# Kernel optimization log

Measured on AMD Instinct MI355X. Metric: run time of the kernel, lower is better.

## Reference

```python
import jax, jax.numpy as jnp
import numpy as np

NUM_CLASSES = 81
THRESHOLD = 0.5
NEGPOS_RATIO = 3
OBJ_SCORE = 0.01
VAR0, VAR1 = 0.1, 0.2


def point_form(boxes):
    # center form (cx,cy,w,h) -> corner form (x1,y1,x2,y2)
    return jnp.concatenate([boxes[:, :2] - boxes[:, 2:] / 2,
                            boxes[:, :2] + boxes[:, 2:] / 2], axis=1)


def jaccard(a, b):
    # a: [A,4] corners, b: [B,4] corners -> IoU [A,B]
    lt = jnp.maximum(a[:, None, :2], b[None, :, :2])
    rb = jnp.minimum(a[:, None, 2:], b[None, :, 2:])
    wh = jnp.clip(rb - lt, 0.0)
    inter = wh[..., 0] * wh[..., 1]
    area_a = ((a[:, 2] - a[:, 0]) * (a[:, 3] - a[:, 1]))[:, None]
    area_b = ((b[:, 2] - b[:, 0]) * (b[:, 3] - b[:, 1]))[None, :]
    return inter / (area_a + area_b - inter)


def encode(matched, priors):
    # matched: [P,4] corner-form GT, priors: [P,4] center-form
    g_cxcy = ((matched[:, :2] + matched[:, 2:]) / 2 - priors[:, :2]) / (VAR0 * priors[:, 2:])
    g_wh = jnp.log((matched[:, 2:] - matched[:, :2]) / priors[:, 2:]) / VAR1
    return jnp.concatenate([g_cxcy, g_wh], axis=1)


def match_one(truths, labels, priors):
    # truths: [O,4] corners, labels: [O] int, priors: [P,4] center-form
    overlaps = jaccard(truths, point_form(priors))      # [O,P]
    best_prior_idx = jnp.argmax(overlaps, axis=1)       # [O]
    best_truth_overlap = jnp.max(overlaps, axis=0)      # [P]
    best_truth_idx = jnp.argmax(overlaps, axis=0)       # [P]
    # ensure every gt matches its best prior
    best_truth_overlap = best_truth_overlap.at[best_prior_idx].set(2.0)
    best_truth_idx = best_truth_idx.at[best_prior_idx].set(jnp.arange(truths.shape[0]))
    matches = truths[best_truth_idx]                    # [P,4]
    conf = jnp.where(best_truth_overlap < THRESHOLD, 0, labels[best_truth_idx].astype(jnp.int32))
    return encode(matches, priors), conf


def smooth_l1(x):
    ax = jnp.abs(x)
    return jnp.where(ax < 1.0, 0.5 * ax * ax, ax - 0.5)


def ce_per_row(logits, tgt):
    # sum-reduction cross-entropy components: logsumexp - logit[target]
    lse = jax.nn.logsumexp(logits, axis=-1)
    picked = jnp.take_along_axis(logits, tgt[..., None].astype(jnp.int32), axis=-1)[..., 0]
    return lse - picked


def setup_inputs() -> dict:
    key = jax.random.key(0)
    ks = jax.random.split(key, 8)
    B, P, O, C = 32, 24564, 16, NUM_CLASSES
    loc_data = jax.random.normal(ks[0], (B, P, 4), jnp.float32)
    conf_data = jax.random.normal(ks[1], (B, P, C), jnp.float32)
    obj_data = jax.random.normal(ks[2], (B, P, 2), jnp.float32)
    # priors in center form
    pc = jax.random.uniform(ks[3], (P, 2), jnp.float32, 0.0, 1.0)
    pwh = jax.random.uniform(ks[4], (P, 2), jnp.float32, 0.05, 0.5)
    priors = jnp.concatenate([pc, pwh], axis=1)
    # gt boxes in corner form, valid (x1<x2, y1<y2)
    tc = jax.random.uniform(ks[5], (B, O, 2), jnp.float32, 0.2, 0.8)
    twh = jax.random.uniform(ks[6], (B, O, 2), jnp.float32, 0.05, 0.3)
    truths = jnp.concatenate([jnp.clip(tc - twh / 2, 0.0, 1.0),
                              jnp.clip(tc + twh / 2, 0.0, 1.0)], axis=-1)
    labels = jax.random.randint(ks[7], (B, O), 1, C).astype(jnp.int64)
    return {"loc_data": loc_data, "conf_data": conf_data, "obj_data": obj_data,
            "priors": priors, "truths": truths, "labels": labels}


def reference(loc_data, conf_data, obj_data, priors, truths, labels):
    num, num_priors = loc_data.shape[:2]
    loc_t, conf_t = jax.vmap(match_one, in_axes=(0, 0, None))(truths, labels, priors)
    loc_t = jax.lax.stop_gradient(loc_t)      # Variable(requires_grad=False)
    conf_t = jax.lax.stop_gradient(conf_t)
    obj_t = (conf_t > 0).astype(jnp.int32)

    obj_conf = jax.lax.stop_gradient(obj_data[:, :, 1])   # .detach()
    pos = conf_t > 0
    # faithful to original (buggy) filter: (pos + neg_positive) > 2 is never true
    neg_positive = (pos.astype(jnp.int32) + (obj_conf < OBJ_SCORE).astype(jnp.int32)) > 2
    pos = pos & ~neg_positive
    pos = jnp.where(pos.sum() == 0, conf_t > 0, pos)

    # localization loss (smooth L1, sum over positives)
    l1 = smooth_l1(loc_data - loc_t).sum(-1)               # [B,P]
    loss_l = jnp.sum(jnp.where(pos, l1, 0.0))

    # objectness loss with hard negative mining
    ce_obj = ce_per_row(obj_data, obj_t)                   # [B,P]
    pos_obj = obj_t > 0
    mining_obj = jnp.where(pos_obj, 0.0, jax.lax.stop_gradient(ce_obj))
    rank_obj = jnp.argsort(jnp.argsort(-mining_obj, axis=1), axis=1)
    num_obj_pos = pos_obj.sum(1, keepdims=True)
    num_obj_neg = jnp.minimum(NEGPOS_RATIO * num_obj_pos, num_priors - 1)
    neg_obj = rank_obj < num_obj_neg
    loss_obj = jnp.sum(jnp.where(pos_obj | neg_obj, ce_obj, 0.0))

    # class confidence loss with hard negative mining
    ce_c = ce_per_row(conf_data, conf_t)                   # [B,P]
    mining_c = jnp.where(pos, 0.0, jax.lax.stop_gradient(ce_c))
    rank_c = jnp.argsort(jnp.argsort(-mining_c, axis=1), axis=1)
    num_pos = pos.sum(1, keepdims=True)
    num_neg = jnp.minimum(NEGPOS_RATIO * num_pos, num_priors - 1)
    neg = rank_c < num_neg
    loss_c = jnp.sum(jnp.where(pos | neg, ce_c, 0.0))

    N = jnp.maximum(num_pos.sum(), 1).astype(loc_data.dtype)
    N1 = jnp.maximum(num_obj_neg.sum(), 1).astype(loc_data.dtype)
    return (loss_l / N, loss_c / N, 0.4 * loss_obj / N1)
```

## Files before the change

### kernel.cpp

```cpp
#include <hip/hip_runtime.h>
#include <hip/hip_bf16.h>
#include <math.h>

#define BB 32
#define PP 24564
#define OO 16
#define CC 81
#define BP (BB * PP)
#define CHUNK 1024

typedef unsigned long long ull;

__device__ __forceinline__ float sl1(float x) {
    float ax = fabsf(x);
    return ax < 1.0f ? 0.5f * ax * ax : ax - 0.5f;
}

__global__ __launch_bounds__(256) void k_match_a(
        const float* __restrict__ priors, const float* __restrict__ truths,
        ull* __restrict__ best_prior ) {
    const int b = blockIdx.y;
    const int p0 = blockIdx.x * CHUNK;
    const int tid = threadIdx.x;
    __shared__ float tr[OO][4];
    __shared__ float tarea[OO];
    __shared__ ull red[4][OO];
    if (tid < OO * 4) ((float*)tr)[tid] = truths[b * OO * 4 + tid];
    __syncthreads();
    if (tid < OO) tarea[tid] = (tr[tid][2] - tr[tid][0]) * (tr[tid][3] - tr[tid][1]);
    __syncthreads();

    float bpv[OO];
    int bpi[OO];
#pragma unroll
    for (int o = 0; o < OO; o++) { bpv[o] = -1.0f; bpi[o] = -1; }

    const int pend = (p0 + CHUNK < PP) ? p0 + CHUNK : PP;
    for (int p = p0 + tid; p < pend; p += 256) {
        const float4 pr = ((const float4*)priors)[p];
        const float x1 = pr.x - pr.z * 0.5f, y1 = pr.y - pr.w * 0.5f;
        const float x2 = pr.x + pr.z * 0.5f, y2 = pr.y + pr.w * 0.5f;
        const float parea = (x2 - x1) * (y2 - y1);
#pragma unroll
        for (int o = 0; o < OO; o++) {
            const float lx = fmaxf(tr[o][0], x1), ly = fmaxf(tr[o][1], y1);
            const float rx = fminf(tr[o][2], x2), ry = fminf(tr[o][3], y2);
            const float iw = fmaxf(rx - lx, 0.0f), ih = fmaxf(ry - ly, 0.0f);
            const float inter = iw * ih;
            const float iou = inter / (tarea[o] + parea - inter);
            if (iou > bpv[o]) { bpv[o] = iou; bpi[o] = p; }
        }
    }

    const int wave = tid >> 6;
    const int lane = tid & 63;
#pragma unroll
    for (int o = 0; o < OO; o++) {
        ull key = (bpi[o] >= 0)
            ? (((ull)__float_as_uint(bpv[o]) << 32) |
               (ull)(0xFFFFFFFFu - (unsigned)bpi[o]))
            : 0ull;
#pragma unroll
        for (int d = 32; d; d >>= 1) {
            const ull other = __shfl_xor(key, d);
            key = (other > key) ? other : key;
        }
        if (lane == 0) red[wave][o] = key;
    }
    __syncthreads();
    if (tid < OO) {
        const ull k0 = red[0][tid], k1 = red[1][tid];
        const ull k2 = red[2][tid], k3 = red[3][tid];
        ull m = k0 > k1 ? k0 : k1;
        const ull m2 = k2 > k3 ? k2 : k3;
        m = m > m2 ? m : m2;
        if (m != 0ull) atomicMax(&best_prior[b * OO + tid], m);
    }
}

__global__ __launch_bounds__(256) void k_ce(
        const float* __restrict__ conf, const float* __restrict__ obj,
        const float* __restrict__ loc, const float* __restrict__ priors,
        const float* __restrict__ truths, const int* __restrict__ labels,
        const ull* __restrict__ best_prior,
        float* __restrict__ mining_obj, float* __restrict__ mining_c,
        int* __restrict__ num_posS ,
        float* __restrict__ accS  ) {
    const int tid = threadIdx.x;
    const int row0 = blockIdx.x * 64;
    const int b0 = row0 / PP;
    __shared__ float sconf[64 * CC];
    __shared__ float slse[64];
    __shared__ float4 s_tr[2][OO];
    __shared__ float  s_ta[2][OO];
    __shared__ int    s_lb[2][OO];
    __shared__ unsigned s_fp[2][OO];

    const int nb = ((row0 - b0 * PP) + 64 > PP) ? 2 : 1;
    if (tid < nb * OO) {
        const int bb = tid >> 4, o = tid & 15;
        const float4 t = ((const float4*)truths)[(b0 + bb) * OO + o];
        s_tr[bb][o] = t;
        s_ta[bb][o] = (t.z - t.x) * (t.w - t.y);
        s_lb[bb][o] = labels[(b0 + bb) * OO + o];
        s_fp[bb][o] = 0xFFFFFFFFu -
            (unsigned)(best_prior[(b0 + bb) * OO + o] & 0xFFFFFFFFull);
    }

    const float4* src = (const float4*)(conf + (size_t)row0 * CC);
    float4* dst = (float4*)sconf;
    for (int i = tid; i < (64 * CC) / 4; i += 256) dst[i] = src[i];
    __syncthreads();

    const int r = tid >> 2;
    const int part = tid & 3;
    const float* rowp = sconf + r * CC;
    const int c0 = part * 20;
    const int c1 = (part == 3) ? CC : c0 + 20;
    float m = -INFINITY;
    for (int c = c0; c < c1; c++) m = fmaxf(m, rowp[c]);
    m = fmaxf(m, __shfl_xor(m, 1));
    m = fmaxf(m, __shfl_xor(m, 2));
    float s = 0.0f;
    for (int c = c0; c < c1; c++) s += __expf(rowp[c] - m);
    s += __shfl_xor(s, 1);
    s += __shfl_xor(s, 2);
    if (part == 0) slse[r] = m + __logf(s);
    __syncthreads();

    if (tid < 64) {
        const int row = row0 + tid;
        const int b = row / PP;
        const int lb_i = b - b0;
        const int p = row - b * PP;

        const float4 pr = ((const float4*)priors)[p];
        const float x1 = pr.x - pr.z * 0.5f, y1 = pr.y - pr.w * 0.5f;
        const float x2 = pr.x + pr.z * 0.5f, y2 = pr.y + pr.w * 0.5f;
        const float parea = (x2 - x1) * (y2 - y1);
        float best = -1.0f;
        int ti = 0;
#pragma unroll
        for (int o = 0; o < OO; o++) {
            const float4 t = s_tr[lb_i][o];
            const float lx = fmaxf(t.x, x1), ly = fmaxf(t.y, y1);
            const float rx = fminf(t.z, x2), ry = fminf(t.w, y2);
            const float iw = fmaxf(rx - lx, 0.0f), ih = fmaxf(ry - ly, 0.0f);
            const float inter = iw * ih;
            const float iou = inter / (s_ta[lb_i][o] + parea - inter);
            if (iou > best) { best = iou; ti = o; }
        }
        float ov = best;
#pragma unroll
        for (int o = 0; o < OO; o++) {
            if (s_fp[lb_i][o] == (unsigned)p) { ti = o; ov = 2.0f; }
        }

        const int lbl = s_lb[lb_i][ti];
        const int tgt = (ov < 0.5f) ? 0 : lbl;
        const float ce_c = slse[tid] - sconf[tid * CC + tgt];

        const float2 o2 = ((const float2*)obj)[row];
        const float mo = fmaxf(o2.x, o2.y);
        const float lse_o = mo + __logf(__expf(o2.x - mo) + __expf(o2.y - mo));
        const bool pos = tgt > 0;
        const float ce_o = lse_o - (pos ? o2.y : o2.x);

        mining_c[row]   = pos ? 0.0f : ce_c;
        mining_obj[row] = pos ? 0.0f : ce_o;

        float my_l = 0.0f, my_co = 0.0f, my_cc = 0.0f;
        if (pos) {
            my_co = ce_o;
            my_cc = ce_c;
            const float4 t = s_tr[lb_i][ti];
            const float gcx = ((t.x + t.z) * 0.5f - pr.x) / (0.1f * pr.z);
            const float gcy = ((t.y + t.w) * 0.5f - pr.y) / (0.1f * pr.w);
            const float gw = logf((t.z - t.x) / pr.z) / 0.2f;
            const float gh = logf((t.w - t.y) / pr.w) / 0.2f;
            const float4 ld = ((const float4*)loc)[row];
            my_l = sl1(ld.x - gcx) + sl1(ld.y - gcy) +
                   sl1(ld.z - gw) + sl1(ld.w - gh);
        }

        const ull mpos = __ballot(pos);
        const ull mb1  = __ballot(b != b0);
#pragma unroll
        for (int d = 32; d; d >>= 1) {
            my_l  += __shfl_down(my_l,  d);
            my_co += __shfl_down(my_co, d);
            my_cc += __shfl_down(my_cc, d);
        }
        if (tid == 0 && mpos) {
            const int cnt0 = __popcll(mpos & ~mb1);
            const int cnt1 = __popcll(mpos &  mb1);
            int* nps = num_posS + (blockIdx.x & 7) * BB;
            if (cnt0) atomicAdd(&nps[b0], cnt0);
            if (cnt1) atomicAdd(&nps[b0 + 1], cnt1);
            float* slot = accS + (size_t)(blockIdx.x & 63) * 32;
            atomicAdd(slot + 0, my_l);
            atomicAdd(slot + 1, my_co);
            atomicAdd(slot + 2, my_cc);
        }
    }
}

__global__ __launch_bounds__(1024) void k_select(
        const float* __restrict__ mining ,
        const int* __restrict__ num_posS ,
        float* __restrict__ acc,
        int* __restrict__ n1_acc) {
    const int arr = blockIdx.x >> 5;
    const int b = blockIdx.x & 31;
    const int tid = threadIdx.x;
    const int wv = tid >> 6;
    const float* x = mining + ((size_t)arr * BB + b) * PP;
    int np = 0;
#pragma unroll
    for (int s = 0; s < 8; s++) np += num_posS[s * BB + b];
    long long k64 = 3LL * np;
    const int k = (int)(k64 < (long long)(PP - 1) ? k64 : (long long)(PP - 1));
    if (tid == 0 && arr == 0) atomicAdd(n1_acc, k);
    if (k <= 0) return;

    __shared__ unsigned histw[16][256];
    __shared__ unsigned hist[256];
    __shared__ unsigned s_prefix;
    __shared__ int s_krem;
    __shared__ float wsum[16];
    __shared__ unsigned wcnt[16];
    if (tid == 0) { s_prefix = 0u; s_krem = k; }

    for (int shift = 24; shift >= 0; shift -= 8) {
        __syncthreads();
        for (int i = tid; i < 16 * 256; i += 1024) ((unsigned*)histw)[i] = 0u;
        const unsigned prefix = s_prefix;
        const unsigned pmask = (shift == 24) ? 0u : (0xFFFFFFFFu << (shift + 8));
        __syncthreads();
        for (int i = tid; i < PP; i += 1024) {
            const unsigned u = __float_as_uint(x[i]);
            if ((u & pmask) == prefix)
                atomicAdd(&histw[wv][(u >> shift) & 255u], 1u);
        }
        __syncthreads();
        if (tid < 256) {
            unsigned s = 0;
#pragma unroll
            for (int w = 0; w < 16; w++) s += histw[w][tid];
            hist[tid] = s;
        }
        __syncthreads();
        if (tid == 0) {
            const int krem = s_krem;
            unsigned cum = 0;
            int sel = 0;
            for (int byte = 255; byte >= 0; byte--) {
                const unsigned h = hist[byte];
                if (cum + h >= (unsigned)krem) { sel = byte; break; }
                cum += h;
            }
            s_krem = krem - (int)cum;
            s_prefix = prefix | ((unsigned)sel << shift);
        }
    }
    __syncthreads();

    const unsigned t = s_prefix;
    float lsum = 0.0f;
    unsigned lcnt = 0;
    for (int i = tid; i < PP; i += 1024) {
        const float v = x[i];
        if (__float_as_uint(v) > t) { lsum += v; lcnt++; }
    }
#pragma unroll
    for (int d = 32; d; d >>= 1) {
        lsum += __shfl_down(lsum, d);
        lcnt += __shfl_down(lcnt, d);
    }
    if ((tid & 63) == 0) { wsum[wv] = lsum; wcnt[wv] = lcnt; }
    __syncthreads();
    if (tid == 0) {
        float ts = 0.0f;
        unsigned tc = 0;
#pragma unroll
        for (int w = 0; w < 16; w++) { ts += wsum[w]; tc += wcnt[w]; }
        const float tsum = ts + (float)(k - (int)tc) * __uint_as_float(t);
        atomicAdd(&acc[3 + arr], tsum);
    }
}

__global__ void k_final(const float* __restrict__ acc,
                        const float* __restrict__ accS ,
                        const int* __restrict__ num_posS ,
                        const int* __restrict__ n1_acc,
                        float* __restrict__ out) {
    const int t = threadIdx.x;
    float sl = accS[t * 32 + 0];
    float so = accS[t * 32 + 1];
    float sc = accS[t * 32 + 2];
    int np = 0;
#pragma unroll
    for (int i = 0; i < 4; i++) np += num_posS[t + i * 64];
#pragma unroll
    for (int d = 32; d; d >>= 1) {
        sl += __shfl_down(sl, d);
        so += __shfl_down(so, d);
        sc += __shfl_down(sc, d);
        np += __shfl_down(np, d);
    }
    if (t == 0) {
        const float fN = (float)(np > 1 ? np : 1);
        const int n1 = *n1_acc;
        const float fN1 = (float)(n1 > 1 ? n1 : 1);
        out[0] = sl / fN;
        out[1] = (sc + acc[4]) / fN;
        out[2] = 0.4f * (so + acc[3]) / fN1;
    }
}

extern "C" void kernel_launch(void* const* d_in, const int* in_sizes, int n_in,
                              void* d_out, int out_size, void* d_ws, size_t ws_size,
                              hipStream_t stream) {
    const float* loc_data  = (const float*)d_in[0];
    const float* conf_data = (const float*)d_in[1];
    const float* obj_data  = (const float*)d_in[2];
    const float* priors    = (const float*)d_in[3];
    const float* truths    = (const float*)d_in[4];
    const int*   labels    = (const int*)d_in[5];
    float* out = (float*)d_out;

    float* ws_f = (float*)d_ws;
    float* mining = ws_f;
    ull*   best_prior = (ull*)(ws_f + 2 * (size_t)BP);
    int*   num_posS = (int*)(ws_f + 2 * (size_t)BP + 1024);
    float* acc = ws_f + 2 * (size_t)BP + 1280;
    int*   n1_acc = (int*)(ws_f + 2 * (size_t)BP + 1288);
    float* accS = ws_f + 2 * (size_t)BP + 2048;

    hipMemsetAsync((void*)best_prior, 0, 16384, stream);

    dim3 mg((PP + CHUNK - 1) / CHUNK, BB);
    k_match_a<<<mg, 256, 0, stream>>>(priors, truths, best_prior);

    k_ce<<<BP / 64, 256, 0, stream>>>(conf_data, obj_data, loc_data, priors,
                                      truths, labels, best_prior,
                                      mining , mining + BP ,
                                      num_posS, accS);

    k_select<<<64, 1024, 0, stream>>>(mining, num_posS, acc, n1_acc);

    k_final<<<1, 64, 0, stream>>>(acc, accS, num_posS, n1_acc, out);
}
```

Measured before the change: 464.7 us.

## Fuse all loss stages into one persistent cooperative kernel with grid syncs

Replaces the four separate launches (match, CE, select, final) with a single cooperative persistent kernel that uses grid.sync between phases. The CE phase now loads conf rows straight into registers instead of staging them in shared memory. The top-k radix select is spread across many blocks using a global histogram and state, where it used to run in only 64 blocks of 1024 threads. This removes launch gaps and the underutilised select phase, at the cost of grid-wide barriers, a larger memset, and lower per-block occupancy limits.

```diff
diff --git a/kernel.cpp b/kernel.cpp
--- a/kernel.cpp
+++ b/kernel.cpp
@@ -1,6 +1,8 @@
 #include <hip/hip_runtime.h>
-#include <hip/hip_bf16.h>
+#include <hip/hip_cooperative_groups.h>
 #include <math.h>
+
+namespace cg = cooperative_groups;
 
 #define BB 32
 #define PP 24564
@@ -8,6 +10,10 @@
 #define CC 81
 #define BP (BB * PP)
 #define CHUNK 1024
+#define NCHK ((PP + CHUNK - 1) / CHUNK)
+#define NMATCH (NCHK * BB)
+#define NTILE (BP / 64)
+#define NSB 512
 
 typedef unsigned long long ull;
 
@@ -16,305 +22,374 @@
     return ax < 1.0f ? 0.5f * ax * ax : ax - 0.5f;
 }
 
-__global__ __launch_bounds__(256) void k_match_a(
-        const float* __restrict__ priors, const float* __restrict__ truths,
-        ull* __restrict__ best_prior ) {
-    const int b = blockIdx.y;
-    const int p0 = blockIdx.x * CHUNK;
-    const int tid = threadIdx.x;
-    __shared__ float tr[OO][4];
-    __shared__ float tarea[OO];
-    __shared__ ull red[4][OO];
-    if (tid < OO * 4) ((float*)tr)[tid] = truths[b * OO * 4 + tid];
-    __syncthreads();
-    if (tid < OO) tarea[tid] = (tr[tid][2] - tr[tid][0]) * (tr[tid][3] - tr[tid][1]);
-    __syncthreads();
-
-    float bpv[OO];
-    int bpi[OO];
-#pragma unroll
-    for (int o = 0; o < OO; o++) { bpv[o] = -1.0f; bpi[o] = -1; }
-
-    const int pend = (p0 + CHUNK < PP) ? p0 + CHUNK : PP;
-    for (int p = p0 + tid; p < pend; p += 256) {
-        const float4 pr = ((const float4*)priors)[p];
-        const float x1 = pr.x - pr.z * 0.5f, y1 = pr.y - pr.w * 0.5f;
-        const float x2 = pr.x + pr.z * 0.5f, y2 = pr.y + pr.w * 0.5f;
-        const float parea = (x2 - x1) * (y2 - y1);
-#pragma unroll
-        for (int o = 0; o < OO; o++) {
-            const float lx = fmaxf(tr[o][0], x1), ly = fmaxf(tr[o][1], y1);
-            const float rx = fminf(tr[o][2], x2), ry = fminf(tr[o][3], y2);
-            const float iw = fmaxf(rx - lx, 0.0f), ih = fmaxf(ry - ly, 0.0f);
-            const float inter = iw * ih;
-            const float iou = inter / (tarea[o] + parea - inter);
-            if (iou > bpv[o]) { bpv[o] = iou; bpi[o] = p; }
-        }
-    }
-
-    const int wave = tid >> 6;
-    const int lane = tid & 63;
-#pragma unroll
-    for (int o = 0; o < OO; o++) {
-        ull key = (bpi[o] >= 0)
-            ? (((ull)__float_as_uint(bpv[o]) << 32) |
-               (ull)(0xFFFFFFFFu - (unsigned)bpi[o]))
-            : 0ull;
-#pragma unroll
-        for (int d = 32; d; d >>= 1) {
-            const ull other = __shfl_xor(key, d);
-            key = (other > key) ? other : key;
-        }
-        if (lane == 0) red[wave][o] = key;
-    }
-    __syncthreads();
-    if (tid < OO) {
-        const ull k0 = red[0][tid], k1 = red[1][tid];
-        const ull k2 = red[2][tid], k3 = red[3][tid];
-        ull m = k0 > k1 ? k0 : k1;
-        const ull m2 = k2 > k3 ? k2 : k3;
-        m = m > m2 ? m : m2;
-        if (m != 0ull) atomicMax(&best_prior[b * OO + tid], m);
-    }
-}
-
-__global__ __launch_bounds__(256) void k_ce(
+__device__ __forceinline__ float4 ld4u(const float* p) {
+    float4 v;
+    __builtin_memcpy(&v, p, 16);
+    return v;
+}
+
+__device__ __forceinline__ float ald(const float* p) {
+    return __hip_atomic_load(p, __ATOMIC_RELAXED, __HIP_MEMORY_SCOPE_AGENT);
+}
+__device__ __forceinline__ int aldi(const int* p) {
+    return __hip_atomic_load(p, __ATOMIC_RELAXED, __HIP_MEMORY_SCOPE_AGENT);
+}
+
+__global__ __launch_bounds__(256, 4) void k_mega(
         const float* __restrict__ conf, const float* __restrict__ obj,
         const float* __restrict__ loc, const float* __restrict__ priors,
         const float* __restrict__ truths, const int* __restrict__ labels,
-        const ull* __restrict__ best_prior,
-        float* __restrict__ mining_obj, float* __restrict__ mining_c,
-        int* __restrict__ num_posS ,
-        float* __restrict__ accS  ) {
+        ull* __restrict__ best_prior,
+        float* __restrict__ mining,
+        int* __restrict__ num_posS,
+        float* __restrict__ acc,
+        float* __restrict__ accS,
+        unsigned* __restrict__ ghist,
+        ull* __restrict__ gstate,
+        float* __restrict__ out) {
     const int tid = threadIdx.x;
-    const int row0 = blockIdx.x * 64;
-    const int b0 = row0 / PP;
-    __shared__ float sconf[64 * CC];
-    __shared__ float slse[64];
-    __shared__ float4 s_tr[2][OO];
-    __shared__ float  s_ta[2][OO];
-    __shared__ int    s_lb[2][OO];
-    __shared__ unsigned s_fp[2][OO];
-
-    const int nb = ((row0 - b0 * PP) + 64 > PP) ? 2 : 1;
-    if (tid < nb * OO) {
-        const int bb = tid >> 4, o = tid & 15;
-        const float4 t = ((const float4*)truths)[(b0 + bb) * OO + o];
-        s_tr[bb][o] = t;
-        s_ta[bb][o] = (t.z - t.x) * (t.w - t.y);
-        s_lb[bb][o] = labels[(b0 + bb) * OO + o];
-        s_fp[bb][o] = 0xFFFFFFFFu -
-            (unsigned)(best_prior[(b0 + bb) * OO + o] & 0xFFFFFFFFull);
-    }
-
-    const float4* src = (const float4*)(conf + (size_t)row0 * CC);
-    float4* dst = (float4*)sconf;
-    for (int i = tid; i < (64 * CC) / 4; i += 256) dst[i] = src[i];
-    __syncthreads();
-
-    const int r = tid >> 2;
-    const int part = tid & 3;
-    const float* rowp = sconf + r * CC;
-    const int c0 = part * 20;
-    const int c1 = (part == 3) ? CC : c0 + 20;
-    float m = -INFINITY;
-    for (int c = c0; c < c1; c++) m = fmaxf(m, rowp[c]);
-    m = fmaxf(m, __shfl_xor(m, 1));
-    m = fmaxf(m, __shfl_xor(m, 2));
-    float s = 0.0f;
-    for (int c = c0; c < c1; c++) s += __expf(rowp[c] - m);
-    s += __shfl_xor(s, 1);
-    s += __shfl_xor(s, 2);
-    if (part == 0) slse[r] = m + __logf(s);
-    __syncthreads();
-
-    if (tid < 64) {
-        const int row = row0 + tid;
+    const int bid = blockIdx.x;
+    const int nblk = gridDim.x;
+    cg::grid_group grid = cg::this_grid();
+
+    __shared__ float s_tr[OO][4];
+    __shared__ float s_ta[OO];
+    __shared__ ull s_red[4][OO];
+    __shared__ unsigned s_histw[4][256];
+    __shared__ unsigned s_bins[256];
+    __shared__ float s_ws[4];
+    __shared__ unsigned s_wc[4];
+
+    for (int task = bid; task < NMATCH; task += nblk) {
+        const int b = task / NCHK;
+        const int c = task - b * NCHK;
+        __syncthreads();
+        if (tid < OO * 4) ((float*)s_tr)[tid] = truths[b * OO * 4 + tid];
+        __syncthreads();
+        if (tid < OO)
+            s_ta[tid] = (s_tr[tid][2] - s_tr[tid][0]) * (s_tr[tid][3] - s_tr[tid][1]);
+        __syncthreads();
+
+        float bpv[OO];
+        int bpi[OO];
+#pragma unroll
+        for (int o = 0; o < OO; o++) { bpv[o] = -1.0f; bpi[o] = -1; }
+
+        const int p0 = c * CHUNK;
+        const int pend = (p0 + CHUNK < PP) ? p0 + CHUNK : PP;
+        for (int p = p0 + tid; p < pend; p += 256) {
+            const float4 pr = ((const float4*)priors)[p];
+            const float x1 = pr.x - pr.z * 0.5f, y1 = pr.y - pr.w * 0.5f;
+            const float x2 = pr.x + pr.z * 0.5f, y2 = pr.y + pr.w * 0.5f;
+            const float parea = (x2 - x1) * (y2 - y1);
+#pragma unroll
+            for (int o = 0; o < OO; o++) {
+                const float lx = fmaxf(s_tr[o][0], x1), ly = fmaxf(s_tr[o][1], y1);
+                const float rx = fminf(s_tr[o][2], x2), ry = fminf(s_tr[o][3], y2);
+                const float iw = fmaxf(rx - lx, 0.0f), ih = fmaxf(ry - ly, 0.0f);
+                const float inter = iw * ih;
+                const float iou = inter / (s_ta[o] + parea - inter);
+                if (iou > bpv[o]) { bpv[o] = iou; bpi[o] = p; }
+            }
+        }
+
+        const int wave = tid >> 6;
+        const int lane = tid & 63;
+#pragma unroll
+        for (int o = 0; o < OO; o++) {
+            ull key = (bpi[o] >= 0)
+                ? (((ull)__float_as_uint(bpv[o]) << 32) |
+                   (ull)(0xFFFFFFFFu - (unsigned)bpi[o]))
+                : 0ull;
+#pragma unroll
+            for (int d = 32; d; d >>= 1) {
+                const ull other = __shfl_xor(key, d);
+                key = (other > key) ? other : key;
+            }
+            if (lane == 0) s_red[wave][o] = key;
+        }
+        __syncthreads();
+        if (tid < OO) {
+            const ull k0 = s_red[0][tid], k1 = s_red[1][tid];
+            const ull k2 = s_red[2][tid], k3 = s_red[3][tid];
+            ull m = k0 > k1 ? k0 : k1;
+            const ull m2 = k2 > k3 ? k2 : k3;
+            m = m > m2 ? m : m2;
+            if (m != 0ull) atomicMax(&best_prior[b * OO + tid], m);
+        }
+    }
+
+    __threadfence();
+    grid.sync();
+
+    for (int tile = bid; tile < NTILE; tile += nblk) {
+        const int row0 = tile * 64;
+        const int r = tid >> 2;
+        const int part = tid & 3;
+        const int row = row0 + r;
+        const float* rowp = conf + (size_t)row * CC;
+        const int c0 = part * 20;
+
+        const float4 v0 = ld4u(rowp + c0);
+        const float4 v1 = ld4u(rowp + c0 + 4);
+        const float4 v2 = ld4u(rowp + c0 + 8);
+        const float4 v3 = ld4u(rowp + c0 + 12);
+        const float4 v4 = ld4u(rowp + c0 + 16);
+        const float ex = (part == 3) ? rowp[80] : 0.0f;
+
+        float m = v0.x;
+        m = fmaxf(m, v0.y); m = fmaxf(m, v0.z); m = fmaxf(m, v0.w);
+        m = fmaxf(m, v1.x); m = fmaxf(m, v1.y); m = fmaxf(m, v1.z); m = fmaxf(m, v1.w);
+        m = fmaxf(m, v2.x); m = fmaxf(m, v2.y); m = fmaxf(m, v2.z); m = fmaxf(m, v2.w);
+        m = fmaxf(m, v3.x); m = fmaxf(m, v3.y); m = fmaxf(m, v3.z); m = fmaxf(m, v3.w);
+        m = fmaxf(m, v4.x); m = fmaxf(m, v4.y); m = fmaxf(m, v4.z); m = fmaxf(m, v4.w);
+        if (part == 3) m = fmaxf(m, ex);
+        m = fmaxf(m, __shfl_xor(m, 1));
+        m = fmaxf(m, __shfl_xor(m, 2));
+
+        float s = 0.0f;
+        s += __expf(v0.x - m); s += __expf(v0.y - m); s += __expf(v0.z - m); s += __expf(v0.w - m);
+        s += __expf(v1.x - m); s += __expf(v1.y - m); s += __expf(v1.z - m); s += __expf(v1.w - m);
+        s += __expf(v2.x - m); s += __expf(v2.y - m); s += __expf(v2.z - m); s += __expf(v2.w - m);
+        s += __expf(v3.x - m); s += __expf(v3.y - m); s += __expf(v3.z - m); s += __expf(v3.w - m);
+        s += __expf(v4.x - m); s += __expf(v4.y - m); s += __expf(v4.z - m); s += __expf(v4.w - m);
+        if (part == 3) s += __expf(ex - m);
+        s += __shfl_xor(s, 1);
+        s += __shfl_xor(s, 2);
+        const float lse = m + __logf(s);
+
         const int b = row / PP;
-        const int lb_i = b - b0;
-        const int p = row - b * PP;
-
-        const float4 pr = ((const float4*)priors)[p];
-        const float x1 = pr.x - pr.z * 0.5f, y1 = pr.y - pr.w * 0.5f;
-        const float x2 = pr.x + pr.z * 0.5f, y2 = pr.y + pr.w * 0.5f;
-        const float parea = (x2 - x1) * (y2 - y1);
-        float best = -1.0f;
-        int ti = 0;
-#pragma unroll
-        for (int o = 0; o < OO; o++) {
-            const float4 t = s_tr[lb_i][o];
-            const float lx = fmaxf(t.x, x1), ly = fmaxf(t.y, y1);
-            const float rx = fminf(t.z, x2), ry = fminf(t.w, y2);
-            const float iw = fmaxf(rx - lx, 0.0f), ih = fmaxf(ry - ly, 0.0f);
-            const float inter = iw * ih;
-            const float iou = inter / (s_ta[lb_i][o] + parea - inter);
-            if (iou > best) { best = iou; ti = o; }
-        }
-        float ov = best;
-#pragma unroll
-        for (int o = 0; o < OO; o++) {
-            if (s_fp[lb_i][o] == (unsigned)p) { ti = o; ov = 2.0f; }
-        }
-
-        const int lbl = s_lb[lb_i][ti];
-        const int tgt = (ov < 0.5f) ? 0 : lbl;
-        const float ce_c = slse[tid] - sconf[tid * CC + tgt];
-
-        const float2 o2 = ((const float2*)obj)[row];
-        const float mo = fmaxf(o2.x, o2.y);
-        const float lse_o = mo + __logf(__expf(o2.x - mo) + __expf(o2.y - mo));
-        const bool pos = tgt > 0;
-        const float ce_o = lse_o - (pos ? o2.y : o2.x);
-
-        mining_c[row]   = pos ? 0.0f : ce_c;
-        mining_obj[row] = pos ? 0.0f : ce_o;
-
+        bool pos = false;
         float my_l = 0.0f, my_co = 0.0f, my_cc = 0.0f;
-        if (pos) {
-            my_co = ce_o;
-            my_cc = ce_c;
-            const float4 t = s_tr[lb_i][ti];
-            const float gcx = ((t.x + t.z) * 0.5f - pr.x) / (0.1f * pr.z);
-            const float gcy = ((t.y + t.w) * 0.5f - pr.y) / (0.1f * pr.w);
-            const float gw = logf((t.z - t.x) / pr.z) / 0.2f;
-            const float gh = logf((t.w - t.y) / pr.w) / 0.2f;
-            const float4 ld = ((const float4*)loc)[row];
-            my_l = sl1(ld.x - gcx) + sl1(ld.y - gcy) +
-                   sl1(ld.z - gw) + sl1(ld.w - gh);
-        }
-
+        if (part == 0) {
+            const int p = row - b * PP;
+            const float4 pr = ((const float4*)priors)[p];
+            const float x1 = pr.x - pr.z * 0.5f, y1 = pr.y - pr.w * 0.5f;
+            const float x2 = pr.x + pr.z * 0.5f, y2 = pr.y + pr.w * 0.5f;
+            const float parea = (x2 - x1) * (y2 - y1);
+            float best = -1.0f;
+            int ti = 0;
+            const float4* trb = (const float4*)truths + b * OO;
+#pragma unroll
+            for (int o = 0; o < OO; o++) {
+                const float4 t = trb[o];
+                const float ta = (t.z - t.x) * (t.w - t.y);
+                const float lx = fmaxf(t.x, x1), ly = fmaxf(t.y, y1);
+                const float rx = fminf(t.z, x2), ry = fminf(t.w, y2);
+                const float iw = fmaxf(rx - lx, 0.0f), ih = fmaxf(ry - ly, 0.0f);
+                const float inter = iw * ih;
+                const float iou = inter / (ta + parea - inter);
+                if (iou > best) { best = iou; ti = o; }
+            }
+            float ov = best;
+#pragma unroll
+            for (int o = 0; o < OO; o++) {
+                const unsigned fp = 0xFFFFFFFFu -
+                    (unsigned)(best_prior[b * OO + o] & 0xFFFFFFFFull);
+                if (fp == (unsigned)p) { ti = o; ov = 2.0f; }
+            }
+
+            const int lbl = labels[b * OO + ti];
+            const int tgt = (ov < 0.5f) ? 0 : lbl;
+            const float ce_c = lse - rowp[tgt];
+
+            const float2 o2 = ((const float2*)obj)[row];
+            const float mo = fmaxf(o2.x, o2.y);
+            const float lse_o = mo + __logf(__expf(o2.x - mo) + __expf(o2.y - mo));
+            pos = tgt > 0;
+            const float ce_o = lse_o - (pos ? o2.y : o2.x);
+
+            mining[BP + row] = pos ? 0.0f : ce_c;
+            mining[row]      = pos ? 0.0f : ce_o;
+
+            if (pos) {
+                my_co = ce_o;
+                my_cc = ce_c;
+                const float4 t = trb[ti];
+                const float gcx = ((t.x + t.z) * 0.5f - pr.x) / (0.1f * pr.z);
+                const float gcy = ((t.y + t.w) * 0.5f - pr.y) / (0.1f * pr.w);
+                const float gw = logf((t.z - t.x) / pr.z) / 0.2f;
+                const float gh = logf((t.w - t.y) / pr.w) / 0.2f;
+                const float4 ld = ((const float4*)loc)[row];
+                my_l = sl1(ld.x - gcx) + sl1(ld.y - gcy) +
+                       sl1(ld.z - gw) + sl1(ld.w - gh);
+            }
+        }
+
+        const int lane = tid & 63;
+        const int w = tid >> 6;
         const ull mpos = __ballot(pos);
-        const ull mb1  = __ballot(b != b0);
+        const int bw0 = __shfl(b, 0);
+        const ull mb1 = __ballot(b != bw0);
 #pragma unroll
         for (int d = 32; d; d >>= 1) {
             my_l  += __shfl_down(my_l,  d);
             my_co += __shfl_down(my_co, d);
             my_cc += __shfl_down(my_cc, d);
         }
-        if (tid == 0 && mpos) {
+        if (lane == 0 && mpos) {
+            const int stripe = tile * 4 + w;
             const int cnt0 = __popcll(mpos & ~mb1);
             const int cnt1 = __popcll(mpos &  mb1);
-            int* nps = num_posS + (blockIdx.x & 7) * BB;
-            if (cnt0) atomicAdd(&nps[b0], cnt0);
-            if (cnt1) atomicAdd(&nps[b0 + 1], cnt1);
-            float* slot = accS + (size_t)(blockIdx.x & 63) * 32;
+            int* nps = num_posS + (stripe & 15) * BB;
+            if (cnt0) atomicAdd(&nps[bw0], cnt0);
+            if (cnt1) atomicAdd(&nps[bw0 + 1], cnt1);
+            float* slot = accS + (size_t)(stripe & 127) * 32;
             atomicAdd(slot + 0, my_l);
             atomicAdd(slot + 1, my_co);
             atomicAdd(slot + 2, my_cc);
         }
     }
-}
-
-__global__ __launch_bounds__(1024) void k_select(
-        const float* __restrict__ mining ,
-        const int* __restrict__ num_posS ,
-        float* __restrict__ acc,
-        int* __restrict__ n1_acc) {
-    const int arr = blockIdx.x >> 5;
-    const int b = blockIdx.x & 31;
-    const int tid = threadIdx.x;
-    const int wv = tid >> 6;
-    const float* x = mining + ((size_t)arr * BB + b) * PP;
-    int np = 0;
-#pragma unroll
-    for (int s = 0; s < 8; s++) np += num_posS[s * BB + b];
-    long long k64 = 3LL * np;
-    const int k = (int)(k64 < (long long)(PP - 1) ? k64 : (long long)(PP - 1));
-    if (tid == 0 && arr == 0) atomicAdd(n1_acc, k);
-    if (k <= 0) return;
-
-    __shared__ unsigned histw[16][256];
-    __shared__ unsigned hist[256];
-    __shared__ unsigned s_prefix;
-    __shared__ int s_krem;
-    __shared__ float wsum[16];
-    __shared__ unsigned wcnt[16];
-    if (tid == 0) { s_prefix = 0u; s_krem = k; }
-
-    for (int shift = 24; shift >= 0; shift -= 8) {
-        __syncthreads();
-        for (int i = tid; i < 16 * 256; i += 1024) ((unsigned*)histw)[i] = 0u;
-        const unsigned prefix = s_prefix;
-        const unsigned pmask = (shift == 24) ? 0u : (0xFFFFFFFFu << (shift + 8));
-        __syncthreads();
-        for (int i = tid; i < PP; i += 1024) {
-            const unsigned u = __float_as_uint(x[i]);
-            if ((u & pmask) == prefix)
-                atomicAdd(&histw[wv][(u >> shift) & 255u], 1u);
-        }
-        __syncthreads();
-        if (tid < 256) {
-            unsigned s = 0;
-#pragma unroll
-            for (int w = 0; w < 16; w++) s += histw[w][tid];
-            hist[tid] = s;
-        }
+
+    __threadfence();
+    grid.sync();
+
+    for (int pass = 0; pass < 4; pass++) {
+        const int shift = 24 - pass * 8;
+        for (int sb = bid; sb < NSB; sb += nblk) {
+            const int task = sb >> 3, sub = sb & 7;
+            const int arr = task >> 5, b = task & 31;
+            unsigned prefix = 0;
+            bool active = true;
+            if (pass > 0) {
+                const ull st = gstate[((pass - 1) & 1) * 64 + task];
+                prefix = (unsigned)(st >> 32);
+                if ((int)(st & 0xFFFFFFFFull) <= 0) active = false;
+            }
+            __syncthreads();
+            for (int i = tid; i < 1024; i += 256) ((unsigned*)s_histw)[i] = 0u;
+            __syncthreads();
+            if (active) {
+                const float* x = mining + ((size_t)arr * BB + b) * PP;
+                const unsigned pmask = (pass == 0) ? 0u : (0xFFFFFFFFu << (shift + 8));
+                const int wv = tid >> 6;
+#pragma unroll
+                for (int j = 0; j < 12; j++) {
+                    const int i = j * 2048 + sub * 256 + tid;
+                    if (i < PP) {
+                        const unsigned u = __float_as_uint(x[i]);
+                        if ((u & pmask) == prefix)
+                            atomicAdd(&s_histw[wv][(u >> shift) & 255u], 1u);
+                    }
+                }
+            }
+            __syncthreads();
+            {
+                const unsigned sum = s_histw[0][tid & 255] + s_histw[1][tid & 255] +
+                                     s_histw[2][tid & 255] + s_histw[3][tid & 255];
+                if (sum) atomicAdd(&ghist[((size_t)pass * 64 + task) * 256 + (tid & 255)], sum);
+            }
+        }
+        __threadfence();
+        grid.sync();
+        for (int sb = bid; sb < NSB; sb += nblk) {
+            const int task = sb >> 3;
+            __syncthreads();
+            s_bins[tid & 255] = ghist[((size_t)pass * 64 + task) * 256 + (tid & 255)];
+            __syncthreads();
+            if (tid == 0) {
+                int krem;
+                unsigned prefix;
+                if (pass == 0) {
+                    const int b = task & 31;
+                    int np = 0;
+#pragma unroll
+                    for (int s2 = 0; s2 < 16; s2++) np += aldi(&num_posS[s2 * BB + b]);
+                    long long k64 = 3LL * np;
+                    krem = (int)(k64 < (long long)(PP - 1) ? k64 : (long long)(PP - 1));
+                    prefix = 0u;
+                } else {
+                    const ull st = gstate[((pass - 1) & 1) * 64 + task];
+                    prefix = (unsigned)(st >> 32);
+                    krem = (int)(st & 0xFFFFFFFFull);
+                }
+                if (krem > 0) {
+                    unsigned cum = 0;
+                    int sel = 0;
+                    for (int byte = 255; byte >= 0; byte--) {
+                        const unsigned h = s_bins[byte];
+                        if (cum + h >= (unsigned)krem) { sel = byte; break; }
+                        cum += h;
+                    }
+                    krem -= (int)cum;
+                    prefix |= (unsigned)sel << shift;
+                }
+                gstate[(pass & 1) * 64 + task] = ((ull)prefix << 32) | (unsigned)krem;
+            }
+        }
+        __syncthreads();
+    }
+    for (int sb = bid; sb < NSB; sb += nblk) {
+        const int task = sb >> 3, sub = sb & 7;
+        const int arr = task >> 5, b = task & 31;
+        int np = 0;
+#pragma unroll
+        for (int s2 = 0; s2 < 16; s2++) np += aldi(&num_posS[s2 * BB + b]);
+        long long k64 = 3LL * np;
+        const int k = (int)(k64 < (long long)(PP - 1) ? k64 : (long long)(PP - 1));
+        if (k <= 0) continue;
+        const unsigned t = (unsigned)(gstate[64 + task] >> 32);
+        const float tf = __uint_as_float(t);
+        const float* x = mining + ((size_t)arr * BB + b) * PP;
+        float lsum = 0.0f;
+        unsigned lcnt = 0;
+#pragma unroll
+        for (int j = 0; j < 12; j++) {
+            const int i = j * 2048 + sub * 256 + tid;
+            if (i < PP) {
+                const float v = x[i];
+                if (__float_as_uint(v) > t) { lsum += v; lcnt++; }
+            }
+        }
+#pragma unroll
+        for (int d = 32; d; d >>= 1) {
+            lsum += __shfl_down(lsum, d);
+            lcnt += __shfl_down(lcnt, d);
+        }
+        const int wv = tid >> 6;
+        __syncthreads();
+        if ((tid & 63) == 0) { s_ws[wv] = lsum; s_wc[wv] = lcnt; }
         __syncthreads();
         if (tid == 0) {
-            const int krem = s_krem;
-            unsigned cum = 0;
-            int sel = 0;
-            for (int byte = 255; byte >= 0; byte--) {
-                const unsigned h = hist[byte];
-                if (cum + h >= (unsigned)krem) { sel = byte; break; }
-                cum += h;
-            }
-            s_krem = krem - (int)cum;
-            s_prefix = prefix | ((unsigned)sel << shift);
-        }
-    }
-    __syncthreads();
-
-    const unsigned t = s_prefix;
-    float lsum = 0.0f;
-    unsigned lcnt = 0;
-    for (int i = tid; i < PP; i += 1024) {
-        const float v = x[i];
-        if (__float_as_uint(v) > t) { lsum += v; lcnt++; }
-    }
-#pragma unroll
-    for (int d = 32; d; d >>= 1) {
-        lsum += __shfl_down(lsum, d);
-        lcnt += __shfl_down(lcnt, d);
-    }
-    if ((tid & 63) == 0) { wsum[wv] = lsum; wcnt[wv] = lcnt; }
-    __syncthreads();
-    if (tid == 0) {
-        float ts = 0.0f;
-        unsigned tc = 0;
-#pragma unroll
-        for (int w = 0; w < 16; w++) { ts += wsum[w]; tc += wcnt[w]; }
-        const float tsum = ts + (float)(k - (int)tc) * __uint_as_float(t);
-        atomicAdd(&acc[3 + arr], tsum);
-    }
-}
-
-__global__ void k_final(const float* __restrict__ acc,
-                        const float* __restrict__ accS ,
-                        const int* __restrict__ num_posS ,
-                        const int* __restrict__ n1_acc,
-                        float* __restrict__ out) {
-    const int t = threadIdx.x;
-    float sl = accS[t * 32 + 0];
-    float so = accS[t * 32 + 1];
-    float sc = accS[t * 32 + 2];
-    int np = 0;
-#pragma unroll
-    for (int i = 0; i < 4; i++) np += num_posS[t + i * 64];
-#pragma unroll
-    for (int d = 32; d; d >>= 1) {
-        sl += __shfl_down(sl, d);
-        so += __shfl_down(so, d);
-        sc += __shfl_down(sc, d);
-        np += __shfl_down(np, d);
-    }
-    if (t == 0) {
-        const float fN = (float)(np > 1 ? np : 1);
-        const int n1 = *n1_acc;
-        const float fN1 = (float)(n1 > 1 ? n1 : 1);
-        out[0] = sl / fN;
-        out[1] = (sc + acc[4]) / fN;
-        out[2] = 0.4f * (so + acc[3]) / fN1;
+            float ts = s_ws[0] + s_ws[1] + s_ws[2] + s_ws[3];
+            const unsigned tc = s_wc[0] + s_wc[1] + s_wc[2] + s_wc[3];
+            float part = ts - (float)(int)tc * tf;
+            if (sub == 0) part += (float)k * tf;
+            atomicAdd(&acc[3 + arr], part);
+        }
+    }
+
+    __threadfence();
+    grid.sync();
+
+    if (bid == 0 && tid < 64) {
+        float sl = ald(&accS[tid * 32 + 0]) + ald(&accS[(tid + 64) * 32 + 0]);
+        float so = ald(&accS[tid * 32 + 1]) + ald(&accS[(tid + 64) * 32 + 1]);
+        float sc = ald(&accS[tid * 32 + 2]) + ald(&accS[(tid + 64) * 32 + 2]);
+        int np_b = 0, k_b = 0;
+        if (tid < BB) {
+#pragma unroll
+            for (int s2 = 0; s2 < 16; s2++) np_b += aldi(&num_posS[s2 * BB + tid]);
+            long long k64 = 3LL * np_b;
+            k_b = (int)(k64 < (long long)(PP - 1) ? k64 : (long long)(PP - 1));
+        }
+#pragma unroll
+        for (int d = 32; d; d >>= 1) {
+            sl += __shfl_down(sl, d);
+            so += __shfl_down(so, d);
+            sc += __shfl_down(sc, d);
+            np_b += __shfl_down(np_b, d);
+            k_b  += __shfl_down(k_b,  d);
+        }
+        if (tid == 0) {
+            const float fN = (float)(np_b > 1 ? np_b : 1);
+            const float fN1 = (float)(k_b > 1 ? k_b : 1);
+            const float a3 = ald(&acc[3]);
+            const float a4 = ald(&acc[4]);
+            out[0] = sl / fN;
+            out[1] = (sc + a4) / fN;
+            out[2] = 0.4f * (so + a3) / fN1;
+        }
     }
 }
 
@@ -331,23 +406,39 @@
 
     float* ws_f = (float*)d_ws;
     float* mining = ws_f;
-    ull*   best_prior = (ull*)(ws_f + 2 * (size_t)BP);
-    int*   num_posS = (int*)(ws_f + 2 * (size_t)BP + 1024);
-    float* acc = ws_f + 2 * (size_t)BP + 1280;
-    int*   n1_acc = (int*)(ws_f + 2 * (size_t)BP + 1288);
-    float* accS = ws_f + 2 * (size_t)BP + 2048;
-
-    hipMemsetAsync((void*)best_prior, 0, 16384, stream);
-
-    dim3 mg((PP + CHUNK - 1) / CHUNK, BB);
-    k_match_a<<<mg, 256, 0, stream>>>(priors, truths, best_prior);
-
-    k_ce<<<BP / 64, 256, 0, stream>>>(conf_data, obj_data, loc_data, priors,
-                                      truths, labels, best_prior,
-                                      mining , mining + BP ,
-                                      num_posS, accS);
-
-    k_select<<<64, 1024, 0, stream>>>(mining, num_posS, acc, n1_acc);
-
-    k_final<<<1, 64, 0, stream>>>(acc, accS, num_posS, n1_acc, out);
-}
+    const size_t S = 2 * (size_t)BP;
+    ull*      best_prior = (ull*)(ws_f + S);
+    int*      num_posS   = (int*)(ws_f + S + 1024);
+    float*    acc        = ws_f + S + 1536;
+    float*    accS       = ws_f + S + 2048;
+    unsigned* ghist      = (unsigned*)(ws_f + S + 6144);
+    ull*      gstate     = (ull*)(ws_f + S + 71680);
+
+    hipMemsetAsync((void*)best_prior, 0, 287744, stream);
+
+    static int s_grid = 0;
+    if (s_grid == 0) {
+        int nb = 0;
+        if (hipOccupancyMaxActiveBlocksPerMultiprocessor(&nb, k_mega, 256, 0)
+                != hipSuccess || nb < 1)
+            nb = 2;
+        int ncu = 256;
+        int dev = 0;
+        hipDeviceProp_t prop;
+        if (hipGetDevice(&dev) == hipSuccess &&
+            hipGetDeviceProperties(&prop, dev) == hipSuccess &&
+            prop.multiProcessorCount > 0)
+            ncu = prop.multiProcessorCount;
+        long long g = (long long)nb * (long long)ncu;
+        s_grid = (int)(g < 1024 ? g : 1024);
+    }
+
+    void* args[] = {
+        (void*)&conf_data, (void*)&obj_data, (void*)&loc_data, (void*)&priors,
+        (void*)&truths, (void*)&labels, (void*)&best_prior, (void*)&mining,
+        (void*)&num_posS, (void*)&acc, (void*)&accS, (void*)&ghist,
+        (void*)&gstate, (void*)&out
+    };
+    hipLaunchCooperativeKernel((void*)k_mega, dim3(s_grid), dim3(256),
+                               args, 0, stream);
+}
```

Result: slower. 1.183 ms (+154.6%).

## Fuse final reduction into select via last-block counter and drop memset

Applied to the files above, without the earlier changes.

Matching now runs one 1024-thread block per batch image, so each block writes its best-prior keys directly and the atomicMax plus hipMemsetAsync are no longer needed. Block 0 of the match kernel zeroes the workspace counters instead. The separate final kernel is folded into the select kernel through a done-counter, where the last block to finish does the final reduction. This removes a memset and one launch but leaves only 32 blocks for matching, which lowers parallelism in that stage.

```diff
diff --git a/kernel.cpp b/kernel.cpp
--- a/kernel.cpp
+++ b/kernel.cpp
@@ -7,7 +7,6 @@
 #define OO 16
 #define CC 81
 #define BP (BB * PP)
-#define CHUNK 1024
 
 typedef unsigned long long ull;
 
@@ -16,15 +15,27 @@
     return ax < 1.0f ? 0.5f * ax * ax : ax - 0.5f;
 }
 
-__global__ __launch_bounds__(256) void k_match_a(
+__device__ __forceinline__ float ald(const float* p) {
+    return __hip_atomic_load(p, __ATOMIC_RELAXED, __HIP_MEMORY_SCOPE_AGENT);
+}
+__device__ __forceinline__ int aldi(const int* p) {
+    return __hip_atomic_load(p, __ATOMIC_RELAXED, __HIP_MEMORY_SCOPE_AGENT);
+}
+
+__global__ __launch_bounds__(1024) void k_match(
         const float* __restrict__ priors, const float* __restrict__ truths,
-        ull* __restrict__ best_prior ) {
-    const int b = blockIdx.y;
-    const int p0 = blockIdx.x * CHUNK;
+        ull* __restrict__ best_prior ,
+        float* __restrict__ zero_base ) {
+    const int b = blockIdx.x;
     const int tid = threadIdx.x;
     __shared__ float tr[OO][4];
     __shared__ float tarea[OO];
-    __shared__ ull red[4][OO];
+    __shared__ ull red[16][OO];
+
+    if (b == 0) {
+        for (int i = tid; i < 3072; i += 1024) zero_base[i] = 0.0f;
+    }
+
     if (tid < OO * 4) ((float*)tr)[tid] = truths[b * OO * 4 + tid];
     __syncthreads();
     if (tid < OO) tarea[tid] = (tr[tid][2] - tr[tid][0]) * (tr[tid][3] - tr[tid][1]);
@@ -35,8 +46,7 @@
 #pragma unroll
     for (int o = 0; o < OO; o++) { bpv[o] = -1.0f; bpi[o] = -1; }
 
-    const int pend = (p0 + CHUNK < PP) ? p0 + CHUNK : PP;
-    for (int p = p0 + tid; p < pend; p += 256) {
+    for (int p = tid; p < PP; p += 1024) {
         const float4 pr = ((const float4*)priors)[p];
         const float x1 = pr.x - pr.z * 0.5f, y1 = pr.y - pr.w * 0.5f;
         const float x2 = pr.x + pr.z * 0.5f, y2 = pr.y + pr.w * 0.5f;
@@ -69,12 +79,13 @@
     }
     __syncthreads();
     if (tid < OO) {
-        const ull k0 = red[0][tid], k1 = red[1][tid];
-        const ull k2 = red[2][tid], k3 = red[3][tid];
-        ull m = k0 > k1 ? k0 : k1;
-        const ull m2 = k2 > k3 ? k2 : k3;
-        m = m > m2 ? m : m2;
-        if (m != 0ull) atomicMax(&best_prior[b * OO + tid], m);
+        ull m = red[0][tid];
+#pragma unroll
+        for (int w = 1; w < 16; w++) {
+            const ull k2 = red[w][tid];
+            m = k2 > m ? k2 : m;
+        }
+        best_prior[b * OO + tid] = m;
     }
 }
 
@@ -205,23 +216,22 @@
     }
 }
 
-__global__ __launch_bounds__(1024) void k_select(
+__global__ __launch_bounds__(1024) void k_select_final(
         const float* __restrict__ mining ,
         const int* __restrict__ num_posS ,
-        float* __restrict__ acc,
-        int* __restrict__ n1_acc) {
+        float* __restrict__ acc ,
+        int* __restrict__ done_ctr,
+        const float* __restrict__ accS ,
+        float* __restrict__ out) {
     const int arr = blockIdx.x >> 5;
     const int b = blockIdx.x & 31;
     const int tid = threadIdx.x;
     const int wv = tid >> 6;
-    const float* x = mining + ((size_t)arr * BB + b) * PP;
     int np = 0;
 #pragma unroll
     for (int s = 0; s < 8; s++) np += num_posS[s * BB + b];
     long long k64 = 3LL * np;
     const int k = (int)(k64 < (long long)(PP - 1) ? k64 : (long long)(PP - 1));
-    if (tid == 0 && arr == 0) atomicAdd(n1_acc, k);
-    if (k <= 0) return;
 
     __shared__ unsigned histw[16][256];
     __shared__ unsigned hist[256];
@@ -229,92 +239,105 @@
     __shared__ int s_krem;
     __shared__ float wsum[16];
     __shared__ unsigned wcnt[16];
-    if (tid == 0) { s_prefix = 0u; s_krem = k; }
-
-    for (int shift = 24; shift >= 0; shift -= 8) {
+    __shared__ int s_last;
+
+    if (k > 0) {
+        const float* x = mining + ((size_t)arr * BB + b) * PP;
+        if (tid == 0) { s_prefix = 0u; s_krem = k; }
+
+        for (int shift = 24; shift >= 0; shift -= 8) {
+            __syncthreads();
+            for (int i = tid; i < 16 * 256; i += 1024) ((unsigned*)histw)[i] = 0u;
+            const unsigned prefix = s_prefix;
+            const unsigned pmask = (shift == 24) ? 0u : (0xFFFFFFFFu << (shift + 8));
+            __syncthreads();
+            for (int i = tid; i < PP; i += 1024) {
+                const unsigned u = __float_as_uint(x[i]);
+                if ((u & pmask) == prefix)
+                    atomicAdd(&histw[wv][(u >> shift) & 255u], 1u);
+            }
+            __syncthreads();
+            if (tid < 256) {
+                unsigned s = 0;
+#pragma unroll
+                for (int w = 0; w < 16; w++) s += histw[w][tid];
+                hist[tid] = s;
+            }
+            __syncthreads();
+            if (tid == 0) {
+                const int krem = s_krem;
+                unsigned cum = 0;
+                int sel = 0;
+                for (int byte = 255; byte >= 0; byte--) {
+                    const unsigned h = hist[byte];
+                    if (cum + h >= (unsigned)krem) { sel = byte; break; }
+                    cum += h;
+                }
+                s_krem = krem - (int)cum;
+                s_prefix = prefix | ((unsigned)sel << shift);
+            }
+        }
         __syncthreads();
-        for (int i = tid; i < 16 * 256; i += 1024) ((unsigned*)histw)[i] = 0u;
-        const unsigned prefix = s_prefix;
-        const unsigned pmask = (shift == 24) ? 0u : (0xFFFFFFFFu << (shift + 8));
-        __syncthreads();
+
+        const unsigned t = s_prefix;
+        float lsum = 0.0f;
+        unsigned lcnt = 0;
         for (int i = tid; i < PP; i += 1024) {
-            const unsigned u = __float_as_uint(x[i]);
-            if ((u & pmask) == prefix)
-                atomicAdd(&histw[wv][(u >> shift) & 255u], 1u);
-        }
-        __syncthreads();
-        if (tid < 256) {
-            unsigned s = 0;
-#pragma unroll
-            for (int w = 0; w < 16; w++) s += histw[w][tid];
-            hist[tid] = s;
-        }
+            const float v = x[i];
+            if (__float_as_uint(v) > t) { lsum += v; lcnt++; }
+        }
+#pragma unroll
+        for (int d = 32; d; d >>= 1) {
+            lsum += __shfl_down(lsum, d);
+            lcnt += __shfl_down(lcnt, d);
+        }
+        if ((tid & 63) == 0) { wsum[wv] = lsum; wcnt[wv] = lcnt; }
         __syncthreads();
         if (tid == 0) {
-            const int krem = s_krem;
-            unsigned cum = 0;
-            int sel = 0;
-            for (int byte = 255; byte >= 0; byte--) {
-                const unsigned h = hist[byte];
-                if (cum + h >= (unsigned)krem) { sel = byte; break; }
-                cum += h;
-            }
-            s_krem = krem - (int)cum;
-            s_prefix = prefix | ((unsigned)sel << shift);
-        }
-    }
-    __syncthreads();
-
-    const unsigned t = s_prefix;
-    float lsum = 0.0f;
-    unsigned lcnt = 0;
-    for (int i = tid; i < PP; i += 1024) {
-        const float v = x[i];
-        if (__float_as_uint(v) > t) { lsum += v; lcnt++; }
-    }
-#pragma unroll
-    for (int d = 32; d; d >>= 1) {
-        lsum += __shfl_down(lsum, d);
-        lcnt += __shfl_down(lcnt, d);
-    }
-    if ((tid & 63) == 0) { wsum[wv] = lsum; wcnt[wv] = lcnt; }
-    __syncthreads();
-    if (tid == 0) {
-        float ts = 0.0f;
-        unsigned tc = 0;
-#pragma unroll
-        for (int w = 0; w < 16; w++) { ts += wsum[w]; tc += wcnt[w]; }
-        const float tsum = ts + (float)(k - (int)tc) * __uint_as_float(t);
-        atomicAdd(&acc[3 + arr], tsum);
-    }
-}
-
-__global__ void k_final(const float* __restrict__ acc,
-                        const float* __restrict__ accS ,
-                        const int* __restrict__ num_posS ,
-                        const int* __restrict__ n1_acc,
-                        float* __restrict__ out) {
-    const int t = threadIdx.x;
-    float sl = accS[t * 32 + 0];
-    float so = accS[t * 32 + 1];
-    float sc = accS[t * 32 + 2];
-    int np = 0;
-#pragma unroll
-    for (int i = 0; i < 4; i++) np += num_posS[t + i * 64];
-#pragma unroll
-    for (int d = 32; d; d >>= 1) {
-        sl += __shfl_down(sl, d);
-        so += __shfl_down(so, d);
-        sc += __shfl_down(sc, d);
-        np += __shfl_down(np, d);
-    }
-    if (t == 0) {
-        const float fN = (float)(np > 1 ? np : 1);
-        const int n1 = *n1_acc;
-        const float fN1 = (float)(n1 > 1 ? n1 : 1);
-        out[0] = sl / fN;
-        out[1] = (sc + acc[4]) / fN;
-        out[2] = 0.4f * (so + acc[3]) / fN1;
+            float ts = 0.0f;
+            unsigned tc = 0;
+#pragma unroll
+            for (int w = 0; w < 16; w++) { ts += wsum[w]; tc += wcnt[w]; }
+            const float tsum = ts + (float)(k - (int)tc) * __uint_as_float(t);
+            atomicAdd(&acc[3 + arr], tsum);
+        }
+    }
+
+    __syncthreads();
+    __threadfence();
+    if (tid == 0) s_last = (atomicAdd(done_ctr, 1) == 63);
+    __syncthreads();
+    if (s_last) {
+        __threadfence();
+        if (tid < 64) {
+            float sl = ald(&accS[tid * 32 + 0]);
+            float so = ald(&accS[tid * 32 + 1]);
+            float sc = ald(&accS[tid * 32 + 2]);
+            int np_b = 0, k_b = 0;
+            if (tid < BB) {
+#pragma unroll
+                for (int s2 = 0; s2 < 8; s2++) np_b += aldi(&num_posS[s2 * BB + tid]);
+                long long kk = 3LL * np_b;
+                k_b = (int)(kk < (long long)(PP - 1) ? kk : (long long)(PP - 1));
+            }
+#pragma unroll
+            for (int d = 32; d; d >>= 1) {
+                sl += __shfl_down(sl, d);
+                so += __shfl_down(so, d);
+                sc += __shfl_down(sc, d);
+                np_b += __shfl_down(np_b, d);
+                k_b  += __shfl_down(k_b,  d);
+            }
+            if (tid == 0) {
+                const float fN = (float)(np_b > 1 ? np_b : 1);
+                const float fN1 = (float)(k_b > 1 ? k_b : 1);
+                const float a3 = ald(&acc[3]);
+                const float a4 = ald(&acc[4]);
+                out[0] = sl / fN;
+                out[1] = (sc + a4) / fN;
+                out[2] = 0.4f * (so + a3) / fN1;
+            }
+        }
     }
 }
 
@@ -331,23 +354,21 @@
 
     float* ws_f = (float*)d_ws;
     float* mining = ws_f;
-    ull*   best_prior = (ull*)(ws_f + 2 * (size_t)BP);
-    int*   num_posS = (int*)(ws_f + 2 * (size_t)BP + 1024);
-    float* acc = ws_f + 2 * (size_t)BP + 1280;
-    int*   n1_acc = (int*)(ws_f + 2 * (size_t)BP + 1288);
-    float* accS = ws_f + 2 * (size_t)BP + 2048;
-
-    hipMemsetAsync((void*)best_prior, 0, 16384, stream);
-
-    dim3 mg((PP + CHUNK - 1) / CHUNK, BB);
-    k_match_a<<<mg, 256, 0, stream>>>(priors, truths, best_prior);
+    const size_t S = 2 * (size_t)BP;
+    ull*   best_prior = (ull*)(ws_f + S);
+    int*   num_posS   = (int*)(ws_f + S + 1024);
+    float* acc        = ws_f + S + 1280;
+    int*   done_ctr   = (int*)(ws_f + S + 1288);
+    float* accS       = ws_f + S + 2048;
+    float* zero_base  = ws_f + S + 1024;
+
+    k_match<<<BB, 1024, 0, stream>>>(priors, truths, best_prior, zero_base);
 
     k_ce<<<BP / 64, 256, 0, stream>>>(conf_data, obj_data, loc_data, priors,
                                       truths, labels, best_prior,
                                       mining , mining + BP ,
                                       num_posS, accS);
 
-    k_select<<<64, 1024, 0, stream>>>(mining, num_posS, acc, n1_acc);
-
-    k_final<<<1, 64, 0, stream>>>(acc, accS, num_posS, n1_acc, out);
-}
+    k_select_final<<<64, 1024, 0, stream>>>(mining, num_posS, acc, done_ctr,
+                                            accS, out);
+}
```

Result: slower. 1.041 ms (+124.1%).
